# Optimization experiments

Measured on AMD Instinct MI355X. Metric: run time of the kernel, lower is better.

Reference implementation:

```python
import jax, jax.numpy as jnp
import numpy as np

H = 256; DS = 8; DC = 4; DI = 512; DTR = 16; NH = 4; EPS = 1e-5
B, N, F, E, S, LC = 8, 512, 32, 8192, 512, 8


def setup_inputs() -> dict:
    key = jax.random.key(0)
    ks = iter(jax.random.split(key, 64))
    def rn(shape, s=0.05):
        return jax.random.normal(next(ks), shape, jnp.float32) * s
    z = lambda *s: jnp.zeros(s, jnp.float32)
    inp = dict(
        node_features=jax.random.normal(next(ks), (B, N, F), jnp.float32),
        edge_index=jax.random.randint(next(ks), (B, 2, E), 0, N),
        W_init=rn((F, H)), b_init=z(H),
        gcn1_W=rn((H, H)), gcn1_b=z(H),
        gcn2_W=rn((H, H)), gcn2_b=z(H),
        in_proj_W=rn((H, 2 * DI)),
        conv_W=rn((DI, DC)), conv_b=z(DI),
        xproj_W=rn((DI, DTR + 2 * DS)),
        dt_W=rn((DTR, DI)), dt_b=z(DI),
        A_log=jnp.log(jnp.tile(jnp.arange(1, DS + 1, dtype=jnp.float32), (DI, 1))),
        Dp=jnp.ones((DI,), jnp.float32),
        out_W=rn((DI, H)),
        Wq=rn((H, H)), bq=z(H), Wk=rn((H, H)), bk=z(H), Wv=rn((H, H)), bv=z(H),
        Wo=rn((H, H)), bo=z(H),
        fus_W=rn((3 * H, H)), fus_b=z(H),
        ln_g=jnp.ones((H,), jnp.float32), ln_b=z(H),
        cw=rn((H, 1)), cb=z(1), hw=rn((H, 4)), hb=z(4), tw=rn((H, 3)), tb=z(3),
        p1w=rn((H, S)), p1b=z(S), p2w=rn((H, S)), p2b=z(S),
        dw=rn((H, S)), db=z(S), sw=rn((H, LC)), sb=z(LC))
    return inp


def gcn(x, src, dst, W, b):
    # PyG GCNConv: self-loops + symmetric deg^{-1/2} normalization, scatter-add.
    n = x.shape[0]
    loops = jnp.arange(n)
    s = jnp.concatenate([src, loops]); d = jnp.concatenate([dst, loops])
    deg = jax.ops.segment_sum(jnp.ones_like(d, x.dtype), d, n)
    dinv = jnp.where(deg > 0, jax.lax.rsqrt(deg), 0.0)
    norm = (dinv[s] * dinv[d])[:, None]
    m = x @ W
    return jax.ops.segment_sum(m[s] * norm, d, n) + b


def mamba(x, in_W, conv_W, conv_b, xproj_W, dt_W, dt_b, A_log, Dp, out_W):
    # mamba_ssm Mamba block, batch=1, seq len L = total nodes.
    L = x.shape[0]
    xz = x @ in_W
    xc, zg = xz[:, :DI], xz[:, DI:]
    xp = jnp.pad(xc, ((DC - 1, 0), (0, 0)))            # causal depthwise conv
    win = xp[jnp.arange(L)[:, None] + jnp.arange(DC)[None, :]]  # [L,K,DI]
    xc = jax.nn.silu(jnp.einsum('lkd,dk->ld', win, conv_W) + conv_b)
    proj = xc @ xproj_W
    dt, Bm, Cm = proj[:, :DTR], proj[:, DTR:DTR + DS], proj[:, DTR + DS:]
    delta = jax.nn.softplus(dt @ dt_W + dt_b)           # [L,DI]
    A = -jnp.exp(A_log)                                 # [DI,DS]
    dA = jnp.exp(delta[:, :, None] * A[None])           # [L,DI,DS]
    dBx = delta[:, :, None] * Bm[:, None, :] * xc[:, :, None]
    def step(h, inp):
        dA_t, dBx_t, C_t = inp
        h = dA_t * h + dBx_t
        return h, (h * C_t[None, :]).sum(-1)
    _, y = jax.lax.scan(step, jnp.zeros((DI, DS), x.dtype), (dA, dBx, Cm))
    y = (y + Dp * xc) * jax.nn.silu(zg)
    return y @ out_W


def mha(x, Wq, bq, Wk, bk, Wv, bv, Wo, bo):
    L = x.shape[0]; hd = H // NH
    q = (x @ Wq + bq).reshape(L, NH, hd)
    k = (x @ Wk + bk).reshape(L, NH, hd)
    v = (x @ Wv + bv).reshape(L, NH, hd)
    s = jnp.einsum('qhd,khd->hqk', q, k) / np.float32(np.sqrt(hd))
    a = jax.nn.softmax(s, axis=-1)
    o = jnp.einsum('hqk,khd->qhd', a, v).reshape(L, H)
    return o @ Wo + bo


def _forward(node_features, edge_index, W_init, b_init, gcn1_W, gcn1_b, gcn2_W, gcn2_b,
             in_proj_W, conv_W, conv_b, xproj_W, dt_W, dt_b, A_log, Dp, out_W,
             Wq, bq, Wk, bk, Wv, bv, Wo, bo, fus_W, fus_b, ln_g, ln_b,
             cw, cb, hw, hb, tw, tb, p1w, p1b, p2w, p2b, dw, db, sw, sb):
    Bsz, Nn, Ff = node_features.shape
    x = node_features.reshape(Bsz * Nn, Ff)
    # offset per-graph edge indices into the flat node space (batching loop)
    ei = (edge_index + (jnp.arange(Bsz) * Nn)[:, None, None]).transpose(1, 0, 2).reshape(2, -1)
    src, dst = ei[0], ei[1]
    h = jax.nn.relu(x @ W_init + b_init)
    h = jax.nn.relu(gcn(h, src, dst, gcn1_W, gcn1_b))
    h = jax.nn.relu(gcn(h, src, dst, gcn2_W, gcn2_b))
    m = mamba(h, in_proj_W, conv_W, conv_b, xproj_W, dt_W, dt_b, A_log, Dp, out_W)
    a = mha(h, Wq, bq, Wk, bk, Wv, bv, Wo, bo)
    fused = jax.nn.relu(jnp.concatenate([h, m, a], -1) @ fus_W + fus_b)
    res = fused + h
    mu = res.mean(-1, keepdims=True)
    var = ((res - mu) ** 2).mean(-1, keepdims=True)
    hf = (res - mu) * jax.lax.rsqrt(var + EPS) * ln_g + ln_b
    batch = jnp.repeat(jnp.arange(Bsz), Nn)
    pooled = jax.ops.segment_sum(hf, batch, Bsz) / jnp.float32(Nn)  # global_mean_pool
    outs = [pooled @ cw + cb, pooled @ hw + hb, pooled @ tw + tb,
            pooled @ p1w + p1b, pooled @ p2w + p2b, pooled @ dw + db,
            pooled @ sw + sb]
    return jnp.concatenate(outs, -1)  # [B, 1+4+3+S+S+S+LC]


def reference(node_features, edge_index, W_init, b_init, gcn1_W, gcn1_b, gcn2_W, gcn2_b,
              in_proj_W, conv_W, conv_b, xproj_W, dt_W, dt_b, A_log, Dp, out_W,
              Wq, bq, Wk, bk, Wv, bv, Wo, bo, fus_W, fus_b, ln_g, ln_b,
              cw, cb, hw, hb, tw, tb, p1w, p1b, p2w, p2b, dw, db, sw, sb):
    return _forward(node_features, edge_index, W_init, b_init, gcn1_W, gcn1_b, gcn2_W, gcn2_b,
                    in_proj_W, conv_W, conv_b, xproj_W, dt_W, dt_b, A_log, Dp, out_W,
                    Wq, bq, Wk, bk, Wv, bv, Wo, bo, fus_W, fus_b, ln_g, ln_b,
                    cw, cb, hw, hb, tw, tb, p1w, p1b, p2w, p2b, dw, db, sw, sb)
```

## Files before the change

### kernel.cpp

```cpp
#include <hip/hip_runtime.h>
#include <hip/hip_bf16.h>
#include <math.h>

typedef __hip_bfloat16 hbf;
typedef short bf16x8 __attribute__((ext_vector_type(8)));
typedef float f32x4 __attribute__((ext_vector_type(4)));

constexpr int NL  = 4096;
constexpr int HH  = 256;
constexpr int NE  = 8192;
constexpr int DIc = 512;
constexpr int DSc = 8;
constexpr int CLc = 16;
constexpr int NOUT = 12416;

constexpr size_t O_MBUF  = 0;
constexpr size_t O_QK    = 1048576;
constexpr size_t O_H2    = 2097152;
constexpr size_t O_CATB  = 3145728;
constexpr size_t O_XZB   = 4718592;
constexpr size_t O_XC    = 6815744;
constexpr size_t O_DELTA = 8912896;
constexpr size_t O_PROJ  = 11010048;
constexpr size_t O_HST   = 11141120;
constexpr size_t O_Y     = 12189696;
constexpr size_t O_POOL  = 13238272;
constexpr size_t O_DINV  = 13240320;
constexpr size_t O_B768  = 13244416;
constexpr size_t O_INT   = 13245184;
constexpr size_t O_WT    = 13327112;
constexpr size_t O_XB    = 13839112;
constexpr size_t O_H0B   = 13904648;
constexpr size_t O_H2B   = 14428936;
constexpr size_t O_XCB   = 14953224;
constexpr size_t O_DTAB  = 16001800;
constexpr size_t O_QKB   = 16067584;
constexpr size_t O_VTB   = 17116160;
constexpr size_t O_PART  = 17640448;
constexpr size_t O_HWT   = 17902592;

constexpr int NW = 12;
__device__ __constant__ int wc_cum[NW+1] = {
    0, 8192, 73728, 139264, 155648, 172032, 303104, 565248,
    630784, 696320, 761856, 827392, 1024000 };
__device__ __constant__ int wc_K [NW] = {32,256,256,512,16,512,256,256,256,256,256,768};
__device__ __constant__ int wc_N [NW] = {256,256,256,32,512,256,1024,256,256,256,256,256};
__device__ __constant__ int wc_Kp[NW] = {32,256,256,512,32,512,256,256,256,256,256,768};
struct WSrc { const float* p[NW]; };
struct HSrc { const float* p[7]; };
struct OPtrs { hbf* p[8]; };

__device__ __constant__ int hw_b[8]  = {0,1,5,8,520,1032,1544,1552};
__device__ __constant__ int hw_nc[7] = {1,4,3,512,512,512,8};

constexpr int PR_W = 1024000;
constexpr int PR_X = PR_W + 131072;
constexpr int PR_B = PR_X + 768;
constexpr int PR_P = PR_B + 262144;
constexpr int PR_I = PR_P + 4096;
constexpr int PR_H = PR_I + 397312;
__global__ __launch_bounds__(256) void prep_k(WSrc ws, hbf* __restrict__ wt,
        const float* __restrict__ x, hbf* __restrict__ xb,
        const float* __restrict__ bq, const float* __restrict__ bk,
        const float* __restrict__ bv,
        float* __restrict__ b768, float* __restrict__ part, int* __restrict__ indeg,
        HSrc hs, float* __restrict__ hwt) {
    int idx = blockIdx.x*256 + threadIdx.x;
    if (idx < PR_W) {
        int lo = 0, hi = NW-1;
        while (lo < hi) { int mid = (lo+hi+1)>>1; if (idx >= wc_cum[mid]) lo = mid; else hi = mid-1; }
        int local = idx - wc_cum[lo];
        int Kp = wc_Kp[lo], K = wc_K[lo], N = wc_N[lo];
        int n = local / Kp, k = local - n*Kp;
        float v = (k < K) ? ws.p[lo][(size_t)k*N + n] : 0.0f;
        wt[idx] = __float2bfloat16(v);
    } else if (idx < PR_X) {
        int i = idx - PR_W;
        xb[i] = __float2bfloat16(x[i]);
    } else if (idx < PR_B) {
        int i = idx - PR_X;
        b768[i] = (i < 256) ? bq[i] : (i < 512 ? bk[i-256] : bv[i-512]);
    } else if (idx < PR_P) {
        part[idx - PR_B] = 0.0f;
    } else if (idx < PR_I) {
        indeg[idx - PR_P] = 0;
    } else if (idx < PR_H) {
        int i = idx - PR_I;
        int j = i >> 8, k = i & 255;
        int seg = 0;
        while (j >= hw_b[seg+1]) seg++;
        int col = j - hw_b[seg], nc = hw_nc[seg];
        hwt[(size_t)j*256 + k] = hs.p[seg][(size_t)k*nc + col];
    }
}

__global__ void count_k(const int* __restrict__ ei, int* __restrict__ indeg) {
    int i = blockIdx.x*256 + threadIdx.x;
    int b = i >> 13, e = i & 8191;
    int dst = ei[b*2*NE + NE + e] + (b << 9);
    atomicAdd(&indeg[dst], 1);
}

__global__ __launch_bounds__(1024) void prefix_k(const int* __restrict__ indeg,
                                                 int* __restrict__ row_start,
                                                 int* __restrict__ cursor,
                                                 float* __restrict__ dinv) {
    __shared__ int part[1024];
    int t = threadIdx.x;
    int v0[4]; int s = 0;
    #pragma unroll
    for (int i = 0; i < 4; i++) {
        int cnt = indeg[t*4 + i];
        v0[i] = s; s += cnt;
        dinv[t*4 + i] = rsqrtf(1.0f + (float)cnt);
    }
    part[t] = s;
    __syncthreads();
    for (int o = 1; o < 1024; o <<= 1) {
        int x = (t >= o) ? part[t-o] : 0;
        __syncthreads();
        part[t] += x;
        __syncthreads();
    }
    int base = (t > 0) ? part[t-1] : 0;
    #pragma unroll
    for (int i = 0; i < 4; i++) {
        int rs = base + v0[i];
        row_start[t*4+i] = rs; cursor[t*4+i] = rs;
    }
    if (t == 1023) row_start[4096] = part[1023];
}

__global__ void scatter_k(const int* __restrict__ ei, int* __restrict__ cursor,
                          int* __restrict__ csr) {
    int i = blockIdx.x*256 + threadIdx.x;
    int b = i >> 13, e = i & 8191;
    int src = ei[b*2*NE + e]       + (b << 9);
    int dst = ei[b*2*NE + NE + e]  + (b << 9);
    int pos = atomicAdd(&cursor[dst], 1);
    csr[pos] = src;
}

template<int MODE>
__global__ __launch_bounds__(256) void gather_k(const float* __restrict__ m,
                        const int* __restrict__ csr, const int* __restrict__ row_start,
                        const float* __restrict__ dinv, const float* __restrict__ bias,
                        float* __restrict__ out, hbf* __restrict__ outb,
                        hbf* __restrict__ catb) {
    int n = blockIdx.x, c = threadIdx.x;
    float dn = dinv[n];
    float acc = m[(size_t)n*HH + c] * dn * dn;
    int e0 = row_start[n], e1 = row_start[n+1];
    for (int e = e0; e < e1; e++) {
        int s = csr[e];
        acc += m[(size_t)s*HH + c] * (dinv[s] * dn);
    }
    float r = fmaxf(acc + bias[c], 0.0f);
    if (MODE) {
        out[(size_t)n*HH + c] = r;
        catb[(size_t)n*768 + c] = __float2bfloat16(r);
    }
    outb[(size_t)n*HH + c] = __float2bfloat16(r);
}

template<int ACT, int OUTM>
__global__ __launch_bounds__(512) void mg_k(const unsigned short* __restrict__ A,
        const unsigned short* __restrict__ Bt, const float* __restrict__ bias,
        void* __restrict__ Cp, int ldc, void* __restrict__ Cp2, void* __restrict__ Cp3,
        const float* __restrict__ resid, int ldr, int M, int K, int N)
{
    __shared__ __align__(16) unsigned short Asm[2][64][40];
    __shared__ __align__(16) unsigned short Bsm[2][64][40];
    int t = threadIdx.x;
    int lane = t & 63, w = t >> 6;
    int wm = w & 3, wn = w >> 2;
    int row0 = blockIdx.x * 64, col0 = blockIdx.y * 64;
    int sr = t >> 3;
    int sk8 = (t & 7) * 8;
    int su = sk8 >> 5, so = sk8 & 31;
    f32x4 acc0 = {}, acc1 = {};
    int fr = lane & 15, fq8 = (lane >> 4) * 8;

    uint4 zz = make_uint4(0u,0u,0u,0u);
    uint4 ra = zz, rb = zz;
    bool bnv = (col0 + sr) < N;
    if (sk8 < K) {
        ra = *(const uint4*)&A[(size_t)(row0+sr)*K + sk8];
        if (bnv) rb = *(const uint4*)&Bt[(size_t)(col0+sr)*K + sk8];
    }

    for (int k0 = 0; k0 < K; k0 += 64) {
        __syncthreads();
        *(uint4*)&Asm[su][sr][so] = ra;
        *(uint4*)&Bsm[su][sr][so] = rb;
        __syncthreads();
        int kn = k0 + 64;
        if (kn < K) {
            ra = rb = zz;
            if (kn + sk8 < K) {
                ra = *(const uint4*)&A[(size_t)(row0+sr)*K + kn + sk8];
                if (bnv) rb = *(const uint4*)&Bt[(size_t)(col0+sr)*K + kn + sk8];
            }
        }
        #pragma unroll
        for (int ks = 0; ks < 2; ks++) {
            bf16x8 a  = *(bf16x8*)&Asm[ks][wm*16 + fr][fq8];
            bf16x8 b0 = *(bf16x8*)&Bsm[ks][wn*32 + fr][fq8];
            bf16x8 b1 = *(bf16x8*)&Bsm[ks][wn*32 + 16 + fr][fq8];
            acc0 = __builtin_amdgcn_mfma_f32_16x16x32_bf16(a, b0, acc0, 0, 0, 0);
            acc1 = __builtin_amdgcn_mfma_f32_16x16x32_bf16(a, b1, acc1, 0, 0, 0);
        }
    }

    int fc = lane & 15, frq = (lane >> 4) * 4;
    if constexpr (OUTM == 4) {
        #pragma unroll
        for (int nt = 0; nt < 2; nt++) {
            int col = col0 + wn*32 + nt*16 + fc;
            if (col >= 32) continue;
            f32x4& av = nt ? acc1 : acc0;
            #pragma unroll
            for (int i = 0; i < 4; i++) {
                int row = row0 + wm*16 + frq + i;
                float v = av[i];
                ((float*)Cp)[(size_t)row*32 + col] = v;
                ((hbf*)Cp2)[(size_t)row*32 + col] = __float2bfloat16((col < 16) ? v : 0.0f);
            }
        }
    } else if constexpr (OUTM == 5) {
        if (col0 < 1024) {
            #pragma unroll
            for (int nt = 0; nt < 2; nt++) {
                int col = col0 + wn*32 + nt*16 + fc;
                f32x4& av = nt ? acc1 : acc0;
                #pragma unroll
                for (int i = 0; i < 4; i++) {
                    int row = row0 + wm*16 + frq + i;
                    ((hbf*)Cp)[(size_t)row*1024 + col] = __float2bfloat16(av[i]);
                }
            }
        } else if (col0 < 1536) {
            #pragma unroll
            for (int nt = 0; nt < 2; nt++) {
                int gcol = col0 + wn*32 + nt*16 + fc;
                int col = gcol - 1024;
                float bvv = bias[col];
                float sc = (col < 256) ? 0.125f : 1.0f;
                f32x4& av = nt ? acc1 : acc0;
                #pragma unroll
                for (int i = 0; i < 4; i++) {
                    int row = row0 + wm*16 + frq + i;
                    ((hbf*)Cp2)[(size_t)row*512 + col] = __float2bfloat16((av[i] + bvv) * sc);
                }
            }
        } else {
            __shared__ __align__(16) unsigned short Ts[64][72];
            #pragma unroll
            for (int nt = 0; nt < 2; nt++) {
                int gcol = col0 + wn*32 + nt*16 + fc;
                float bvv = bias[gcol - 1024];
                f32x4& av = nt ? acc1 : acc0;
                #pragma unroll
                for (int i = 0; i < 4; i++)
                    *(hbf*)&Ts[wn*32 + nt*16 + fc][wm*16 + frq + i] = __float2bfloat16(av[i] + bvv);
            }
            __syncthreads();
            int c = t >> 3, rs = (t & 7) * 8;
            *(uint4*)((hbf*)Cp3 + (size_t)(col0 - 1536 + c)*NL + row0 + rs) = *(uint4*)&Ts[c][rs];
        }
    } else {
        #pragma unroll
        for (int nt = 0; nt < 2; nt++) {
            int col = col0 + wn*32 + nt*16 + fc;
            if (col >= N) continue;
            float bvv = bias ? bias[col] : 0.0f;
            f32x4& av = nt ? acc1 : acc0;
            #pragma unroll
            for (int i = 0; i < 4; i++) {
                int row = row0 + wm*16 + frq + i;
                float v = av[i] + bvv;
                if (ACT == 1) v = fmaxf(v, 0.0f);
                if (ACT == 2) v = (v > 20.0f) ? v : log1pf(expf(v));
                if (resid) v += resid[(size_t)row*ldr + col];
                if (OUTM == 0) ((float*)Cp)[(size_t)row*ldc + col] = v;
                else           ((hbf*)Cp)[(size_t)row*ldc + col] = __float2bfloat16(v);
            }
        }
    }
}

__global__ void conv_k(const hbf* __restrict__ xzb, const float* __restrict__ cW,
                       const float* __restrict__ cb, hbf* __restrict__ xcb) {
    int i = blockIdx.x*256 + threadIdx.x;
    int l = i >> 9, d = i & 511;
    float acc = cb[d];
    #pragma unroll
    for (int k = 0; k < 4; k++) {
        int ls = l - 3 + k;
        if (ls >= 0) acc += __bfloat162float(xzb[(size_t)ls*1024 + d]) * cW[d*4 + k];
    }
    float r = acc / (1.0f + __expf(-acc));
    xcb[i] = __float2bfloat16(r);
}

__global__ __launch_bounds__(256) void scan1_k(const float* __restrict__ delta,
                        const hbf* __restrict__ xc, const float* __restrict__ proj,
                        const float* __restrict__ Alog,
                        float* __restrict__ P, float* __restrict__ Hl)
{
    int c = blockIdx.x >> 1;
    int d = ((blockIdx.x & 1) << 8) + threadIdx.x;
    float Ac[DSc], pr[DSc], h[DSc];
    #pragma unroll
    for (int s2 = 0; s2 < DSc; s2++) { Ac[s2] = -__expf(Alog[d*DSc+s2]); pr[s2]=1.0f; h[s2]=0.0f; }
    int l0 = c * CLc;
    for (int l = l0; l < l0 + CLc; l++) {
        float dl = delta[(size_t)l*DIc + d];
        float dx = dl * __bfloat162float(xc[(size_t)l*DIc + d]);
        const float* pb = proj + l*32 + 16;
        #pragma unroll
        for (int s2 = 0; s2 < DSc; s2++) {
            float a = __expf(dl * Ac[s2]);
            h[s2] = a*h[s2] + dx*pb[s2];
            pr[s2] *= a;
        }
    }
    #pragma unroll
    for (int s2 = 0; s2 < DSc; s2++) {
        P [(size_t)(c*DSc+s2)*DIc + d] = pr[s2];
        Hl[(size_t)(c*DSc+s2)*DIc + d] = h[s2];
    }
}

__global__ __launch_bounds__(256) void scan2t_k(const float* __restrict__ P,
                        const float* __restrict__ Hl, float* __restrict__ Hst) {
    __shared__ float Ps[256][17], Hs[256][17];
    int t = threadIdx.x, sg = blockIdx.x;
    int si = t & 15, cb = t >> 4;
    #pragma unroll
    for (int it = 0; it < 16; it++) {
        int c = it*16 + cb;
        size_t off = (size_t)c*4096 + sg*16 + si;
        Ps[c][si] = P[off];
        Hs[c][si] = Hl[off];
    }
    __syncthreads();
    int si2 = t >> 4, g = t & 15;
    int lane = t & 63;
    float Pg = 1.0f, Hg = 0.0f;
    #pragma unroll
    for (int j = 0; j < 16; j++) {
        int c = g*16 + j;
        float pc = Ps[c][si2], hc = Hs[c][si2];
        Hg = hc + pc*Hg;
        Pg = pc*Pg;
    }
    #pragma unroll
    for (int off = 1; off < 16; off <<= 1) {
        float Pp = __shfl(Pg, lane - off);
        float Hp = __shfl(Hg, lane - off);
        if (g >= off) { Hg = Hg + Pg*Hp; Pg = Pg*Pp; }
    }
    float carry = __shfl(Hg, lane - 1);
    if (g == 0) carry = 0.0f;
    float h = carry;
    #pragma unroll
    for (int j = 0; j < 16; j++) {
        int c = g*16 + j;
        float pc = Ps[c][si2], hc = Hs[c][si2];
        Hs[c][si2] = h;
        h = hc + pc*h;
    }
    __syncthreads();
    #pragma unroll
    for (int it = 0; it < 16; it++) {
        int c = it*16 + cb;
        Hst[(size_t)c*4096 + sg*16 + si] = Hs[c][si];
    }
}

__global__ __launch_bounds__(256) void scan3_k(const float* __restrict__ delta,
                        const hbf* __restrict__ xc, const float* __restrict__ proj,
                        const float* __restrict__ Alog, const float* __restrict__ Hst,
                        const float* __restrict__ Dp, const hbf* __restrict__ xzb,
                        hbf* __restrict__ Y)
{
    int c = blockIdx.x >> 1;
    int d = ((blockIdx.x & 1) << 8) + threadIdx.x;
    float Ac[DSc], h[DSc];
    #pragma unroll
    for (int s2 = 0; s2 < DSc; s2++) {
        Ac[s2] = -__expf(Alog[d*DSc+s2]);
        h[s2]  = Hst[(size_t)(c*DSc+s2)*DIc + d];
    }
    float dpv = Dp[d];
    int l0 = c * CLc;
    for (int l = l0; l < l0 + CLc; l++) {
        float dl = delta[(size_t)l*DIc + d];
        float xv = __bfloat162float(xc[(size_t)l*DIc + d]);
        float dx = dl * xv;
        const float* pb = proj + l*32 + 16;
        float y = 0.0f;
        #pragma unroll
        for (int s2 = 0; s2 < DSc; s2++) {
            float a = __expf(dl * Ac[s2]);
            h[s2] = a*h[s2] + dx*pb[s2];
            y += h[s2] * pb[8+s2];
        }
        float z = __bfloat162float(xzb[(size_t)l*1024 + 512 + d]);
        float sz = z / (1.0f + __expf(-z));
        Y[(size_t)l*DIc + d] = __float2bfloat16((y + dpv*xv) * sz);
    }
}

__global__ __launch_bounds__(256) void attn_part_k(const unsigned short* __restrict__ QK,
                       const unsigned short* __restrict__ Vt,
                       OPtrs op, float* __restrict__ lsum)
{
    __shared__ __align__(16) unsigned short QPs[128][72];
    __shared__ __align__(16) unsigned short Ks[64][72];
    __shared__ __align__(16) unsigned short Vs[64][72];
    int t = threadIdx.x, lane = t & 63, w = t >> 6;
    int h = blockIdx.y, q0 = blockIdx.x * 128, skc = blockIdx.z;
    int fm = lane & 15, fq = lane >> 4;

    {
        int qr = t >> 1, qc = (t & 1) * 32;
        const unsigned short* src = &QK[(size_t)(q0+qr)*512 + h*64 + qc];
        *(uint4*)&QPs[qr][qc]      = *(const uint4*)&src[0];
        *(uint4*)&QPs[qr][qc + 8]  = *(const uint4*)&src[8];
        *(uint4*)&QPs[qr][qc + 16] = *(const uint4*)&src[16];
        *(uint4*)&QPs[qr][qc + 24] = *(const uint4*)&src[24];
    }
    __syncthreads();
    bf16x8 qa[2][2];
    #pragma unroll
    for (int rf = 0; rf < 2; rf++)
        #pragma unroll
        for (int ks = 0; ks < 2; ks++)
            qa[rf][ks] = *(bf16x8*)&QPs[w*32 + rf*16 + fm][ks*32 + fq*8];

    bf16x8 ones;
    #pragma unroll
    for (int j = 0; j < 8; j++) ones[j] = (short)0x3F80;

    f32x4 o[2][4] = {};
    f32x4 ol[2] = {};
    int sr = t >> 2, sk = (t & 3) * 16;
    const unsigned short* Kb = QK + 256;
    int kt = skc * 512;
    uint4 ka  = *(const uint4*)&Kb[(size_t)(kt+sr)*512 + h*64 + sk];
    uint4 kb2 = *(const uint4*)&Kb[(size_t)(kt+sr)*512 + h*64 + sk + 8];
    uint4 va  = *(const uint4*)&Vt[(size_t)(h*64+sr)*NL + kt + sk];
    uint4 vb2 = *(const uint4*)&Vt[(size_t)(h*64+sr)*NL + kt + sk + 8];

    for (int it = 0; it < 8; it++) {
        __syncthreads();
        *(uint4*)&Ks[sr][sk] = ka;  *(uint4*)&Ks[sr][sk+8] = kb2;
        *(uint4*)&Vs[sr][sk] = va;  *(uint4*)&Vs[sr][sk+8] = vb2;
        __syncthreads();
        if (it < 7) {
            int kn = kt + 64;
            ka  = *(const uint4*)&Kb[(size_t)(kn+sr)*512 + h*64 + sk];
            kb2 = *(const uint4*)&Kb[(size_t)(kn+sr)*512 + h*64 + sk + 8];
            va  = *(const uint4*)&Vt[(size_t)(h*64+sr)*NL + kn + sk];
            vb2 = *(const uint4*)&Vt[(size_t)(h*64+sr)*NL + kn + sk + 8];
        }
        f32x4 s[2][4] = {};
        #pragma unroll
        for (int ks = 0; ks < 2; ks++) {
            #pragma unroll
            for (int nt = 0; nt < 4; nt++) {
                bf16x8 kb = *(bf16x8*)&Ks[nt*16 + fm][ks*32 + fq*8];
                s[0][nt] = __builtin_amdgcn_mfma_f32_16x16x32_bf16(qa[0][ks], kb, s[0][nt], 0, 0, 0);
                s[1][nt] = __builtin_amdgcn_mfma_f32_16x16x32_bf16(qa[1][ks], kb, s[1][nt], 0, 0, 0);
            }
        }
        #pragma unroll
        for (int rf = 0; rf < 2; rf++)
            #pragma unroll
            for (int nt = 0; nt < 4; nt++)
                #pragma unroll
                for (int i = 0; i < 4; i++) {
                    float p = __expf(s[rf][nt][i] - 4.0f);
                    *(hbf*)&QPs[w*32 + rf*16 + fq*4 + i][nt*16 + fm] = __float2bfloat16(p);
                }
        #pragma unroll
        for (int ks = 0; ks < 2; ks++) {
            bf16x8 pa0 = *(bf16x8*)&QPs[w*32 + fm][ks*32 + fq*8];
            bf16x8 pa1 = *(bf16x8*)&QPs[w*32 + 16 + fm][ks*32 + fq*8];
            #pragma unroll
            for (int nt = 0; nt < 4; nt++) {
                bf16x8 vb = *(bf16x8*)&Vs[nt*16 + fm][ks*32 + fq*8];
                o[0][nt] = __builtin_amdgcn_mfma_f32_16x16x32_bf16(pa0, vb, o[0][nt], 0, 0, 0);
                o[1][nt] = __builtin_amdgcn_mfma_f32_16x16x32_bf16(pa1, vb, o[1][nt], 0, 0, 0);
            }
            ol[0] = __builtin_amdgcn_mfma_f32_16x16x32_bf16(pa0, ones, ol[0], 0, 0, 0);
            ol[1] = __builtin_amdgcn_mfma_f32_16x16x32_bf16(pa1, ones, ol[1], 0, 0, 0);
        }
        kt += 64;
    }
    hbf* Op = op.p[skc];
    #pragma unroll
    for (int rf = 0; rf < 2; rf++)
        #pragma unroll
        for (int i = 0; i < 4; i++) {
            int row = w*32 + rf*16 + fq*4 + i;
            #pragma unroll
            for (int nt = 0; nt < 4; nt++)
                Op[(size_t)(q0 + row)*HH + h*64 + nt*16 + fm] = __float2bfloat16(o[rf][nt][i]);
        }
    if (fm == 0) {
        #pragma unroll
        for (int rf = 0; rf < 2; rf++)
            #pragma unroll
            for (int i = 0; i < 4; i++)
                lsum[(size_t)(skc*4 + h)*NL + q0 + w*32 + rf*16 + fq*4 + i] = ol[rf][i];
    }
}

__global__ __launch_bounds__(256) void amerge_k(OPtrs op, const float* __restrict__ lsum,
                                                hbf* __restrict__ aob) {
    int row = blockIdx.x, t = threadIdx.x, h = t >> 6;
    float L = 0.0f, s = 0.0f;
    #pragma unroll
    for (int c = 0; c < 8; c++) {
        L += lsum[(size_t)(c*4 + h)*NL + row];
        s += __bfloat162float(op.p[c][(size_t)row*HH + t]);
    }
    aob[(size_t)row*HH + t] = __float2bfloat16(s / L);
}

__global__ __launch_bounds__(256) void ln_k(const float* __restrict__ X,
                    const float* __restrict__ g, const float* __restrict__ b,
                    float* __restrict__ part) {
    __shared__ float red[4];
    int r = blockIdx.x, t = threadIdx.x;
    float v = X[(size_t)r*HH + t];
    float s = v;
    #pragma unroll
    for (int o = 32; o > 0; o >>= 1) s += __shfl_down(s, o);
    if ((t & 63) == 0) red[t >> 6] = s;
    __syncthreads();
    float mean = (red[0]+red[1]+red[2]+red[3]) * (1.0f/256.0f);
    float dfv = v - mean;
    float s2 = dfv*dfv;
    #pragma unroll
    for (int o = 32; o > 0; o >>= 1) s2 += __shfl_down(s2, o);
    __syncthreads();
    if ((t & 63) == 0) red[t >> 6] = s2;
    __syncthreads();
    float var = (red[0]+red[1]+red[2]+red[3]) * (1.0f/256.0f);
    float y = dfv * rsqrtf(var + 1e-5f) * g[t] + b[t];
    atomicAdd(&part[(size_t)(r & 127)*2048 + (r >> 9)*HH + t], y * (1.0f/512.0f));
}

__global__ void reduce_k(const float* __restrict__ part, float* __restrict__ pooled) {
    int i = blockIdx.x*256 + threadIdx.x;
    float s = 0.0f;
    #pragma unroll 8
    for (int p = 0; p < 128; p++) s += part[(size_t)p*2048 + i];
    pooled[i] = s;
}

__global__ __launch_bounds__(256) void heads_k(const float* __restrict__ pooled,
        const float* __restrict__ hwt,
        const float* cbh, const float* hb, const float* tb, const float* p1b,
        const float* p2b, const float* db, const float* sb, float* __restrict__ out)
{
    int idx = blockIdx.x*4 + (threadIdx.x >> 6);
    int lane = threadIdx.x & 63;
    if (idx >= NOUT) return;
    int b = idx / 1552, j = idx - b*1552;
    const float* bi; int col;
    if (j < 1)         { bi = cbh; col = j;        }
    else if (j < 5)    { bi = hb;  col = j - 1;    }
    else if (j < 8)    { bi = tb;  col = j - 5;    }
    else if (j < 520)  { bi = p1b; col = j - 8;    }
    else if (j < 1032) { bi = p2b; col = j - 520;  }
    else if (j < 1544) { bi = db;  col = j - 1032; }
    else               { bi = sb;  col = j - 1544; }
    const float* pl = pooled + b*HH;
    const float* wr = hwt + (size_t)j*256;
    float s = 0.0f;
    #pragma unroll
    for (int k = lane; k < 256; k += 64) s = fmaf(pl[k], wr[k], s);
    #pragma unroll
    for (int o = 32; o > 0; o >>= 1) s += __shfl_down(s, o);
    if (lane == 0) out[idx] = s + bi[col];
}

extern "C" void kernel_launch(void* const* d_in, const int* in_sizes, int n_in,
                              void* d_out, int out_size, void* d_ws, size_t ws_size,
                              hipStream_t stream)
{
    (void)in_sizes; (void)n_in; (void)out_size; (void)ws_size;
    const float* x      = (const float*)d_in[0];
    const int*   ei     = (const int*)  d_in[1];
    const float* W_init = (const float*)d_in[2];
    const float* b_init = (const float*)d_in[3];
    const float* g1W = (const float*)d_in[4];
    const float* g1b = (const float*)d_in[5];
    const float* g2W = (const float*)d_in[6];
    const float* g2b = (const float*)d_in[7];
    const float* inW = (const float*)d_in[8];
    const float* cW  = (const float*)d_in[9];
    const float* cb  = (const float*)d_in[10];
    const float* xpW = (const float*)d_in[11];
    const float* dtW = (const float*)d_in[12];
    const float* dtb = (const float*)d_in[13];
    const float* Alog= (const float*)d_in[14];
    const float* Dp  = (const float*)d_in[15];
    const float* outW= (const float*)d_in[16];
    const float* Wq  = (const float*)d_in[17];
    const float* bq  = (const float*)d_in[18];
    const float* Wk  = (const float*)d_in[19];
    const float* bk  = (const float*)d_in[20];
    const float* Wv  = (const float*)d_in[21];
    const float* bv  = (const float*)d_in[22];
    const float* Wo  = (const float*)d_in[23];
    const float* bo  = (const float*)d_in[24];
    const float* fusW= (const float*)d_in[25];
    const float* fusb= (const float*)d_in[26];
    const float* lng = (const float*)d_in[27];
    const float* lnb = (const float*)d_in[28];
    const float* cwp = (const float*)d_in[29];
    const float* cbp = (const float*)d_in[30];
    const float* hwp = (const float*)d_in[31];
    const float* hbp = (const float*)d_in[32];
    const float* twp = (const float*)d_in[33];
    const float* tbp = (const float*)d_in[34];
    const float* p1w = (const float*)d_in[35];
    const float* p1b = (const float*)d_in[36];
    const float* p2w = (const float*)d_in[37];
    const float* p2b = (const float*)d_in[38];
    const float* dwp = (const float*)d_in[39];
    const float* dbp = (const float*)d_in[40];
    const float* swp = (const float*)d_in[41];
    const float* sbp = (const float*)d_in[42];

    float* fw = (float*)d_ws;
    int* iw = (int*)(fw + O_INT);
    int* indeg = iw;
    int* row_start = iw + 4096;
    int* cursor = iw + 8193;
    int* csr = iw + 12289;
    float* dinv = fw + O_DINV;

    hbf* wt   = (hbf*)(fw + O_WT);
    hbf* xb   = (hbf*)(fw + O_XB);
    hbf* h0b  = (hbf*)(fw + O_H0B);
    hbf* h2b  = (hbf*)(fw + O_H2B);
    hbf* xcb  = (hbf*)(fw + O_XCB);
    hbf* dtab = (hbf*)(fw + O_DTAB);
    hbf* xzb  = (hbf*)(fw + O_XZB);
    hbf* yb   = (hbf*)(fw + O_Y);
    hbf* aob  = (hbf*)(fw + O_Y);
    hbf* catb = (hbf*)(fw + O_CATB);
    hbf* qkB  = (hbf*)(fw + O_QKB);
    hbf* vtB  = (hbf*)(fw + O_VTB);
    float* fused = fw + O_XC;
    float* b768 = fw + O_B768;
    float* part = fw + O_PART;
    float* hwt  = fw + O_HWT;

    float* scanP  = fw + O_MBUF;
    float* scanHl = fw + O_QK;
    float* scanHst= fw + O_HST;
    float* lsum   = fw + O_HST;

    OPtrs op;
    op.p[0] = (hbf*)(fw + O_MBUF);
    op.p[1] = (hbf*)(fw + O_MBUF + 524288);
    op.p[2] = (hbf*)(fw + O_DELTA);
    op.p[3] = (hbf*)(fw + O_DELTA + 524288);
    op.p[4] = (hbf*)(fw + O_DELTA + 1048576);
    op.p[5] = (hbf*)(fw + O_DELTA + 1572864);
    op.p[6] = (hbf*)(fw + O_XZB);
    op.p[7] = (hbf*)(fw + O_XZB + 524288);

    hbf* WtInit  = wt + 0;
    hbf* WtG1    = wt + 8192;
    hbf* WtG2    = wt + 73728;
    hbf* WtXp    = wt + 139264;
    hbf* WtDt    = wt + 155648;
    hbf* WtOut   = wt + 172032;
    hbf* WtInQKV = wt + 303104;
    hbf* WtO     = wt + 761856;
    hbf* WtFus   = wt + 827392;

    WSrc wsrc;
    wsrc.p[0]=W_init; wsrc.p[1]=g1W; wsrc.p[2]=g2W; wsrc.p[3]=xpW; wsrc.p[4]=dtW;
    wsrc.p[5]=outW; wsrc.p[6]=inW; wsrc.p[7]=Wq; wsrc.p[8]=Wk; wsrc.p[9]=Wv;
    wsrc.p[10]=Wo; wsrc.p[11]=fusW;
    HSrc hsrc;
    hsrc.p[0]=cwp; hsrc.p[1]=hwp; hsrc.p[2]=twp; hsrc.p[3]=p1w;
    hsrc.p[4]=p2w; hsrc.p[5]=dwp; hsrc.p[6]=swp;
    prep_k<<<(PR_H+255)/256,256,0,stream>>>(wsrc, wt, x, xb, bq, bk, bv, b768,
                                            part, indeg, hsrc, hwt);

    count_k<<<256,256,0,stream>>>(ei, indeg);
    prefix_k<<<1,1024,0,stream>>>(indeg, row_start, cursor, dinv);
    scatter_k<<<256,256,0,stream>>>(ei, cursor, csr);

    mg_k<1,1><<<dim3(64,4),512,0,stream>>>((const unsigned short*)xb, (const unsigned short*)WtInit,
        b_init, h0b, 256, nullptr, nullptr, nullptr, 0, NL, 32, 256);
    mg_k<0,0><<<dim3(64,4),512,0,stream>>>((const unsigned short*)h0b, (const unsigned short*)WtG1,
        nullptr, fw+O_MBUF, 256, nullptr, nullptr, nullptr, 0, NL, 256, 256);
    gather_k<0><<<4096,256,0,stream>>>(fw+O_MBUF, csr, row_start, dinv, g1b, nullptr, h0b, nullptr);
    mg_k<0,0><<<dim3(64,4),512,0,stream>>>((const unsigned short*)h0b, (const unsigned short*)WtG2,
        nullptr, fw+O_MBUF, 256, nullptr, nullptr, nullptr, 0, NL, 256, 256);
    gather_k<1><<<4096,256,0,stream>>>(fw+O_MBUF, csr, row_start, dinv, g2b, fw+O_H2, h2b, catb);

    mg_k<0,5><<<dim3(64,28),512,0,stream>>>((const unsigned short*)h2b, (const unsigned short*)WtInQKV,
        b768, xzb, 1024, qkB, vtB, nullptr, 0, NL, 256, 1792);

    conv_k<<<8192,256,0,stream>>>(xzb, cW, cb, xcb);
    mg_k<0,4><<<dim3(64,1),512,0,stream>>>((const unsigned short*)xcb, (const unsigned short*)WtXp,
        nullptr, fw+O_PROJ, 32, dtab, nullptr, nullptr, 0, NL, 512, 32);
    mg_k<2,0><<<dim3(64,8),512,0,stream>>>((const unsigned short*)dtab, (const unsigned short*)WtDt,
        dtb, fw+O_DELTA, 512, nullptr, nullptr, nullptr, 0, NL, 32, 512);
    scan1_k<<<512,256,0,stream>>>(fw+O_DELTA, xcb, fw+O_PROJ, Alog, scanP, scanHl);
    scan2t_k<<<256,256,0,stream>>>(scanP, scanHl, scanHst);
    scan3_k<<<512,256,0,stream>>>(fw+O_DELTA, xcb, fw+O_PROJ, Alog, scanHst, Dp, xzb, yb);
    mg_k<0,1><<<dim3(64,4),512,0,stream>>>((const unsigned short*)yb, (const unsigned short*)WtOut,
        nullptr, catb + 256, 768, nullptr, nullptr, nullptr, 0, NL, 512, 256);

    attn_part_k<<<dim3(32,4,8),256,0,stream>>>((const unsigned short*)qkB,
        (const unsigned short*)vtB, op, lsum);
    amerge_k<<<4096,256,0,stream>>>(op, lsum, aob);
    mg_k<0,1><<<dim3(64,4),512,0,stream>>>((const unsigned short*)aob, (const unsigned short*)WtO,
        bo, catb + 512, 768, nullptr, nullptr, nullptr, 0, NL, 256, 256);

    mg_k<1,0><<<dim3(64,4),512,0,stream>>>((const unsigned short*)catb, (const unsigned short*)WtFus,
        fusb, fused, 256, nullptr, nullptr, fw+O_H2, 256, NL, 768, 256);
    ln_k<<<4096,256,0,stream>>>(fused, lng, lnb, part);
    reduce_k<<<8,256,0,stream>>>(part, fw+O_POOL);
    heads_k<<<(NOUT+3)/4,256,0,stream>>>(fw+O_POOL, hwt, cbp,hbp,tbp,p1b,p2b,dbp,sbp,
                                         (float*)d_out);
}
```

Measured before the change: 353.5 us.

## Use 8 waves per attention block with 16 query rows each

The attention partial kernel goes from 4 waves of 32 query rows each to 8 waves of 16 query rows each, in 512-thread blocks, with the cooperative Q/K/V tile loads split across twice as many threads. This halves per-wave accumulator registers and adds waves per CU to hide LDS and MFMA latency. In exchange, each wave does half the MFMA work per loaded K/V fragment, so there is less register reuse of K/V fragments and more block-wide sync participants.

```diff
diff --git a/kernel.cpp b/kernel.cpp
--- a/kernel.cpp
+++ b/kernel.cpp
@@ -413,7 +413,7 @@
     }
 }
 
-__global__ __launch_bounds__(256) void attn_part_k(const unsigned short* __restrict__ QK,
+__global__ __launch_bounds__(512, 8) void attn_part_k(const unsigned short* __restrict__ QK,
                        const unsigned short* __restrict__ Vt,
                        OPtrs op, float* __restrict__ lsum)
 {
@@ -425,97 +425,79 @@
     int fm = lane & 15, fq = lane >> 4;
 
     {
-        int qr = t >> 1, qc = (t & 1) * 32;
+        int qr = t >> 2, qc = (t & 3) * 16;
         const unsigned short* src = &QK[(size_t)(q0+qr)*512 + h*64 + qc];
-        *(uint4*)&QPs[qr][qc]      = *(const uint4*)&src[0];
-        *(uint4*)&QPs[qr][qc + 8]  = *(const uint4*)&src[8];
-        *(uint4*)&QPs[qr][qc + 16] = *(const uint4*)&src[16];
-        *(uint4*)&QPs[qr][qc + 24] = *(const uint4*)&src[24];
+        *(uint4*)&QPs[qr][qc]     = *(const uint4*)&src[0];
+        *(uint4*)&QPs[qr][qc + 8] = *(const uint4*)&src[8];
     }
     __syncthreads();
-    bf16x8 qa[2][2];
-    #pragma unroll
-    for (int rf = 0; rf < 2; rf++)
-        #pragma unroll
-        for (int ks = 0; ks < 2; ks++)
-            qa[rf][ks] = *(bf16x8*)&QPs[w*32 + rf*16 + fm][ks*32 + fq*8];
+    bf16x8 qa[2];
+    #pragma unroll
+    for (int ks = 0; ks < 2; ks++)
+        qa[ks] = *(bf16x8*)&QPs[w*16 + fm][ks*32 + fq*8];
 
     bf16x8 ones;
     #pragma unroll
     for (int j = 0; j < 8; j++) ones[j] = (short)0x3F80;
 
-    f32x4 o[2][4] = {};
-    f32x4 ol[2] = {};
-    int sr = t >> 2, sk = (t & 3) * 16;
+    f32x4 o[4] = {};
+    f32x4 ol = {};
+    int sr = t >> 3, sk = (t & 7) * 8;
     const unsigned short* Kb = QK + 256;
     int kt = skc * 512;
-    uint4 ka  = *(const uint4*)&Kb[(size_t)(kt+sr)*512 + h*64 + sk];
-    uint4 kb2 = *(const uint4*)&Kb[(size_t)(kt+sr)*512 + h*64 + sk + 8];
-    uint4 va  = *(const uint4*)&Vt[(size_t)(h*64+sr)*NL + kt + sk];
-    uint4 vb2 = *(const uint4*)&Vt[(size_t)(h*64+sr)*NL + kt + sk + 8];
+    uint4 ka = *(const uint4*)&Kb[(size_t)(kt+sr)*512 + h*64 + sk];
+    uint4 va = *(const uint4*)&Vt[(size_t)(h*64+sr)*NL + kt + sk];
 
     for (int it = 0; it < 8; it++) {
         __syncthreads();
-        *(uint4*)&Ks[sr][sk] = ka;  *(uint4*)&Ks[sr][sk+8] = kb2;
-        *(uint4*)&Vs[sr][sk] = va;  *(uint4*)&Vs[sr][sk+8] = vb2;
+        *(uint4*)&Ks[sr][sk] = ka;
+        *(uint4*)&Vs[sr][sk] = va;
         __syncthreads();
         if (it < 7) {
             int kn = kt + 64;
-            ka  = *(const uint4*)&Kb[(size_t)(kn+sr)*512 + h*64 + sk];
-            kb2 = *(const uint4*)&Kb[(size_t)(kn+sr)*512 + h*64 + sk + 8];
-            va  = *(const uint4*)&Vt[(size_t)(h*64+sr)*NL + kn + sk];
-            vb2 = *(const uint4*)&Vt[(size_t)(h*64+sr)*NL + kn + sk + 8];
-        }
-        f32x4 s[2][4] = {};
+            ka = *(const uint4*)&Kb[(size_t)(kn+sr)*512 + h*64 + sk];
+            va = *(const uint4*)&Vt[(size_t)(h*64+sr)*NL + kn + sk];
+        }
+        f32x4 s[4] = {};
         #pragma unroll
         for (int ks = 0; ks < 2; ks++) {
             #pragma unroll
             for (int nt = 0; nt < 4; nt++) {
                 bf16x8 kb = *(bf16x8*)&Ks[nt*16 + fm][ks*32 + fq*8];
-                s[0][nt] = __builtin_amdgcn_mfma_f32_16x16x32_bf16(qa[0][ks], kb, s[0][nt], 0, 0, 0);
-                s[1][nt] = __builtin_amdgcn_mfma_f32_16x16x32_bf16(qa[1][ks], kb, s[1][nt], 0, 0, 0);
-            }
-        }
-        #pragma unroll
-        for (int rf = 0; rf < 2; rf++)
+                s[nt] = __builtin_amdgcn_mfma_f32_16x16x32_bf16(qa[ks], kb, s[nt], 0, 0, 0);
+            }
+        }
+        #pragma unroll
+        for (int nt = 0; nt < 4; nt++)
             #pragma unroll
-            for (int nt = 0; nt < 4; nt++)
-                #pragma unroll
-                for (int i = 0; i < 4; i++) {
-                    float p = __expf(s[rf][nt][i] - 4.0f);
-                    *(hbf*)&QPs[w*32 + rf*16 + fq*4 + i][nt*16 + fm] = __float2bfloat16(p);
-                }
+            for (int i = 0; i < 4; i++) {
+                float p = __expf(s[nt][i] - 4.0f);
+                *(hbf*)&QPs[w*16 + fq*4 + i][nt*16 + fm] = __float2bfloat16(p);
+            }
         #pragma unroll
         for (int ks = 0; ks < 2; ks++) {
-            bf16x8 pa0 = *(bf16x8*)&QPs[w*32 + fm][ks*32 + fq*8];
-            bf16x8 pa1 = *(bf16x8*)&QPs[w*32 + 16 + fm][ks*32 + fq*8];
+            bf16x8 pa = *(bf16x8*)&QPs[w*16 + fm][ks*32 + fq*8];
             #pragma unroll
             for (int nt = 0; nt < 4; nt++) {
                 bf16x8 vb = *(bf16x8*)&Vs[nt*16 + fm][ks*32 + fq*8];
-                o[0][nt] = __builtin_amdgcn_mfma_f32_16x16x32_bf16(pa0, vb, o[0][nt], 0, 0, 0);
-                o[1][nt] = __builtin_amdgcn_mfma_f32_16x16x32_bf16(pa1, vb, o[1][nt], 0, 0, 0);
-            }
-            ol[0] = __builtin_amdgcn_mfma_f32_16x16x32_bf16(pa0, ones, ol[0], 0, 0, 0);
-            ol[1] = __builtin_amdgcn_mfma_f32_16x16x32_bf16(pa1, ones, ol[1], 0, 0, 0);
+                o[nt] = __builtin_amdgcn_mfma_f32_16x16x32_bf16(pa, vb, o[nt], 0, 0, 0);
+            }
+            ol = __builtin_amdgcn_mfma_f32_16x16x32_bf16(pa, ones, ol, 0, 0, 0);
         }
         kt += 64;
     }
     hbf* Op = op.p[skc];
     #pragma unroll
-    for (int rf = 0; rf < 2; rf++)
-        #pragma unroll
-        for (int i = 0; i < 4; i++) {
-            int row = w*32 + rf*16 + fq*4 + i;
-            #pragma unroll
-            for (int nt = 0; nt < 4; nt++)
-                Op[(size_t)(q0 + row)*HH + h*64 + nt*16 + fm] = __float2bfloat16(o[rf][nt][i]);
-        }
+    for (int i = 0; i < 4; i++) {
+        int row = w*16 + fq*4 + i;
+        #pragma unroll
+        for (int nt = 0; nt < 4; nt++)
+            Op[(size_t)(q0 + row)*HH + h*64 + nt*16 + fm] = __float2bfloat16(o[nt][i]);
+    }
     if (fm == 0) {
         #pragma unroll
-        for (int rf = 0; rf < 2; rf++)
-            #pragma unroll
-            for (int i = 0; i < 4; i++)
-                lsum[(size_t)(skc*4 + h)*NL + q0 + w*32 + rf*16 + fq*4 + i] = ol[rf][i];
+        for (int i = 0; i < 4; i++)
+            lsum[(size_t)(skc*4 + h)*NL + q0 + w*16 + fq*4 + i] = ol[i];
     }
 }
 
@@ -726,7 +708,7 @@
     mg_k<0,1><<<dim3(64,4),512,0,stream>>>((const unsigned short*)yb, (const unsigned short*)WtOut,
         nullptr, catb + 256, 768, nullptr, nullptr, nullptr, 0, NL, 512, 256);
 
-    attn_part_k<<<dim3(32,4,8),256,0,stream>>>((const unsigned short*)qkB,
+    attn_part_k<<<dim3(32,4,8),512,0,stream>>>((const unsigned short*)qkB,
         (const unsigned short*)vtB, op, lsum);
     amerge_k<<<4096,256,0,stream>>>(op, lsum, aob);
     mg_k<0,1><<<dim3(64,4),512,0,stream>>>((const unsigned short*)aob, (const unsigned short*)WtO,
```

New measurement: 353.8 us. About the same (+0.1%).
